# Performance work log

Hardware: AMD Instinct MI355X
Metric: run time of the kernel (lower is better)

The kernel has to match this reference:

```python
import jax, jax.numpy as jnp
import numpy as np

N_STEPS = 4  # fixed-step dopri5 substeps over [t0, t1]
T0, T1 = 0.0, 1.0
EPS = 1e-5

# Dormand-Prince 5(4) Butcher tableau (5th-order solution weights)
_DP_A = [
    [],
    [1/5],
    [3/40, 9/40],
    [44/45, -56/15, 32/9],
    [19372/6561, -25360/2187, 64448/6561, -212/729],
    [9017/3168, -355/33, 46732/5247, 49/176, -5103/18656],
    [35/384, 0.0, 500/1113, 125/192, -2187/6784, 11/84],
]
_DP_B = [35/384, 0.0, 500/1113, 125/192, -2187/6784, 11/84, 0.0]


def _layernorm(x, g, b):
    mu = jnp.mean(x, axis=-1, keepdims=True)
    var = jnp.var(x, axis=-1, keepdims=True)
    return (x - mu) * jax.lax.rsqrt(var + EPS) * g + b


def build_laplacian(edge_index, edge_attr, num_nodes, ew_w1, ew_b1, ew_w2, ew_b2):
    # learnable edge weights: Linear(1,32) -> ReLU -> Linear(32,1) -> Sigmoid
    h = jax.nn.relu(edge_attr @ ew_w1 + ew_b1)            # [E,32]
    ew = jax.nn.sigmoid(h @ ew_w2 + ew_b2)[:, 0]           # [E]
    row, col = edge_index[0], edge_index[1]
    # add self loops with weight 1
    loop = jnp.arange(num_nodes, dtype=edge_index.dtype)
    row = jnp.concatenate([row, loop])
    col = jnp.concatenate([col, loop])
    ew = jnp.concatenate([ew, jnp.ones((num_nodes,), dtype=ew.dtype)])
    # degree counts edges incident on col (unweighted, as torch_geometric.degree)
    deg = jnp.zeros((num_nodes,), dtype=ew.dtype).at[col].add(1.0)
    dis = jnp.where(deg > 0, deg ** -0.5, 0.0)
    w = dis[row] * ew * dis[col]
    adj = jnp.zeros((num_nodes, num_nodes), dtype=ew.dtype).at[row, col].add(w)
    return jnp.eye(num_nodes, dtype=ew.dtype) - adj


def ode_func(state, L, context, p):
    # state: [B,N,F], L: [N,N], context: [B,F]
    B, N, F = state.shape
    ctx = jnp.broadcast_to(context[:, None, :], (B, N, F))
    x = jnp.concatenate([state, ctx], axis=-1)             # [B,N,2F]
    h = jax.nn.relu(_layernorm(x @ p['td_w1'] + p['td_b1'], p['ln1_g'], p['ln1_b']))
    h = jax.nn.relu(_layernorm(h @ p['td_w2'] + p['td_b2'], p['ln2_g'], p['ln2_b']))
    dhdt_temporal = h @ p['td_w3'] + p['td_b3']            # [B,N,F]
    dcoef = jax.nn.sigmoid(jax.nn.relu(state @ p['df_w1'] + p['df_b1']) @ p['df_w2'] + p['df_b2'])  # [B,N,1]
    Lh = jnp.einsum('ij,bjf->bif', L, state)               # batched diffusion
    return dhdt_temporal - dcoef * Lh


def dopri5_fixed(f, y0, t0, t1, n_steps):
    dt = (t1 - t0) / n_steps

    def step(y, _):
        ks = []
        for i in range(7):
            yi = y
            for j, aij in enumerate(_DP_A[i]):
                if aij != 0.0:
                    yi = yi + dt * aij * ks[j]
            ks.append(f(yi))
        ynew = y
        for bi, ki in zip(_DP_B, ks):
            if bi != 0.0:
                ynew = ynew + dt * bi * ki
        return ynew, None

    y, _ = jax.lax.scan(step, y0, None, length=n_steps)
    return y


def setup_inputs() -> dict:
    key = jax.random.key(0)
    ks = jax.random.split(key, 24)
    B, N, F, H, E = 4, 2048, 256, 512, 65536
    s = lambda k, *shape: jax.random.normal(k, shape, dtype=jnp.float32) * 0.05
    return {
        'state': jax.random.normal(ks[0], (B, N, F), dtype=jnp.float32),
        'context': jax.random.normal(ks[1], (B, F), dtype=jnp.float32),
        'edge_attr': jax.random.uniform(ks[2], (E, 1), dtype=jnp.float32),
        'edge_index': jax.random.randint(ks[3], (2, E), 0, N, dtype=jnp.int32),
        'ew_w1': s(ks[4], 1, 32), 'ew_b1': jnp.zeros((32,), jnp.float32),
        'ew_w2': s(ks[5], 32, 1), 'ew_b2': jnp.zeros((1,), jnp.float32),
        'td_w1': s(ks[6], 2 * F, H), 'td_b1': jnp.zeros((H,), jnp.float32),
        'ln1_g': jnp.ones((H,), jnp.float32), 'ln1_b': jnp.zeros((H,), jnp.float32),
        'td_w2': s(ks[7], H, H), 'td_b2': jnp.zeros((H,), jnp.float32),
        'ln2_g': jnp.ones((H,), jnp.float32), 'ln2_b': jnp.zeros((H,), jnp.float32),
        'td_w3': s(ks[8], H, F), 'td_b3': jnp.zeros((F,), jnp.float32),
        'df_w1': s(ks[9], F, H // 2), 'df_b1': jnp.zeros((H // 2,), jnp.float32),
        'df_w2': s(ks[10], H // 2, 1), 'df_b2': jnp.zeros((1,), jnp.float32),
    }


def reference(state, context, edge_attr, edge_index,
              ew_w1, ew_b1, ew_w2, ew_b2,
              td_w1, td_b1, ln1_g, ln1_b, td_w2, td_b2, ln2_g, ln2_b, td_w3, td_b3,
              df_w1, df_b1, df_w2, df_b2):
    N = state.shape[1]
    L = build_laplacian(edge_index, edge_attr, N, ew_w1, ew_b1, ew_w2, ew_b2)
    p = dict(td_w1=td_w1, td_b1=td_b1, ln1_g=ln1_g, ln1_b=ln1_b,
             td_w2=td_w2, td_b2=td_b2, ln2_g=ln2_g, ln2_b=ln2_b,
             td_w3=td_w3, td_b3=td_b3, df_w1=df_w1, df_b1=df_b1,
             df_w2=df_w2, df_b2=df_b2)
    f = lambda y: ode_func(y, L, context, p)
    return dopri5_fixed(f, state, T0, T1, N_STEPS)
```

## Files before the change

### kernel.cpp

```cpp
#include <hip/hip_runtime.h>
#include <cstddef>
#include <cstdint>

#define N_NODES 2048
#define BATCH   4
#define FDIM    256
#define HDIM    512
#define NEDGE   65536
#define BN_     8192
#define DT      0.25f

typedef __attribute__((ext_vector_type(8))) __bf16 bf16x8;
typedef __attribute__((ext_vector_type(4))) float f32x4;

__device__ __forceinline__ ushort f2bf(float f) {
    union { float f; unsigned u; } v; v.f = f;
    return (ushort)((v.u + 0x7FFF + ((v.u >> 16) & 1)) >> 16);
}
__device__ __forceinline__ float bf2f(ushort u) {
    union { float f; unsigned u; } v; v.u = ((unsigned)u) << 16; return v.f;
}
__device__ __forceinline__ void gload16(const void* g, void* l) {
    __builtin_amdgcn_global_load_lds((const __attribute__((address_space(1))) void*)g,
                                     (__attribute__((address_space(3))) void*)l, 16, 0, 0);
}

__global__ void edge_ew_deg(const float* __restrict__ attr, const int* __restrict__ eidx,
                            const float* __restrict__ w1, const float* __restrict__ b1,
                            const float* __restrict__ w2, const float* __restrict__ b2,
                            float* __restrict__ ew, float* __restrict__ deg) {
    int e = blockIdx.x * blockDim.x + threadIdx.x;
    if (e >= NEDGE) return;
    float a = attr[e];
    float s = b2[0];
#pragma unroll
    for (int k = 0; k < 32; ++k)
        s += fmaxf(fmaf(a, w1[k], b1[k]), 0.f) * w2[k];
    ew[e] = 1.f / (1.f + expf(-s));
    atomicAdd(&deg[eidx[NEDGE + e]], 1.f);
}

__global__ void dis_diag(const float* __restrict__ deg, float* __restrict__ dis,
                         float* __restrict__ L) {
    int n = blockIdx.x * blockDim.x + threadIdx.x;
    if (n >= N_NODES) return;
    float d = deg[n] + 1.f;
    dis[n] = rsqrtf(d);
    L[(size_t)n * N_NODES + n] = 1.f - 1.f / d;
}

__global__ void scatter_L(const int* __restrict__ eidx, const float* __restrict__ ew,
                          const float* __restrict__ dis, float* __restrict__ L) {
    int e = blockIdx.x * blockDim.x + threadIdx.x;
    if (e >= NEDGE) return;
    int r = eidx[e], c = eidx[NEDGE + e];
    atomicAdd(&L[(size_t)r * N_NODES + c], -dis[r] * ew[e] * dis[c]);
}

__global__ void ctxproj_kernel(const float* __restrict__ ctx, const float* __restrict__ w1,
                               const float* __restrict__ b1, float* __restrict__ out) {
    int b = blockIdx.x, h = threadIdx.x;
    const float* W = w1 + (size_t)FDIM * HDIM + h;
    const float* c = ctx + b * FDIM;
    float s = b1[h];
#pragma unroll 4
    for (int k = 0; k < FDIM; ++k)
        s = fmaf(c[k], W[(size_t)k * HDIM], s);
    out[b * HDIM + h] = s;
}

__global__ __launch_bounds__(256)
void transpose_cvt(const float* __restrict__ in, int inStride, ushort* __restrict__ out,
                   int R, int C) {
    __shared__ float tile[64][65];
    int r0 = blockIdx.x * 64, c0 = blockIdx.y * 64;
    int t = threadIdx.x, tr = t >> 4, tc = t & 15;
#pragma unroll
    for (int i = 0; i < 4; ++i) {
        float4 v = *(const float4*)&in[(size_t)(r0 + tr + i * 16) * inStride + c0 + tc * 4];
        tile[tr + i * 16][tc * 4 + 0] = v.x; tile[tr + i * 16][tc * 4 + 1] = v.y;
        tile[tr + i * 16][tc * 4 + 2] = v.z; tile[tr + i * 16][tc * 4 + 3] = v.w;
    }
    __syncthreads();
#pragma unroll
    for (int i = 0; i < 4; ++i) {
        int c = tr + i * 16;
        ushort4 o = make_ushort4(f2bf(tile[tc * 4 + 0][c]), f2bf(tile[tc * 4 + 1][c]),
                                 f2bf(tile[tc * 4 + 2][c]), f2bf(tile[tc * 4 + 3][c]));
        *(ushort4*)&out[(size_t)(c0 + c) * R + r0 + tc * 4] = o;
    }
}

__global__ void cvt_bf16(const float* __restrict__ in, ushort* __restrict__ out) {
    int i = blockIdx.x * blockDim.x + threadIdx.x;
    float4 v = ((const float4*)in)[i];
    ((ushort4*)out)[i] = make_ushort4(f2bf(v.x), f2bf(v.y), f2bf(v.z), f2bf(v.w));
}

__global__ __launch_bounds__(256)
void combine_all(const float* __restrict__ base,
                 const ushort* p0, const ushort* p1, const ushort* p2,
                 const ushort* p3, const ushort* p4,
                 float c0, float c1, float c2, float c3, float c4,
                 float* __restrict__ dstf, ushort* __restrict__ yi,
                 ushort* __restrict__ yiT) {
    __shared__ ushort tile[64][68];
    int nb = blockIdx.x * 64, fb = blockIdx.y * 64, b = blockIdx.z;
    int t = threadIdx.x, tr = t >> 4, tc = t & 15;
#pragma unroll
    for (int i = 0; i < 4; ++i) {
        int nl = tr + i * 16;
        size_t fi = (((size_t)(b * N_NODES + nb + nl) * FDIM) + fb + tc * 4) >> 2;
        float4 v = ((const float4*)base)[fi];
        if (p0) { ushort4 q = ((const ushort4*)p0)[fi]; v.x = fmaf(c0,bf2f(q.x),v.x); v.y = fmaf(c0,bf2f(q.y),v.y); v.z = fmaf(c0,bf2f(q.z),v.z); v.w = fmaf(c0,bf2f(q.w),v.w); }
        if (p1) { ushort4 q = ((const ushort4*)p1)[fi]; v.x = fmaf(c1,bf2f(q.x),v.x); v.y = fmaf(c1,bf2f(q.y),v.y); v.z = fmaf(c1,bf2f(q.z),v.z); v.w = fmaf(c1,bf2f(q.w),v.w); }
        if (p2) { ushort4 q = ((const ushort4*)p2)[fi]; v.x = fmaf(c2,bf2f(q.x),v.x); v.y = fmaf(c2,bf2f(q.y),v.y); v.z = fmaf(c2,bf2f(q.z),v.z); v.w = fmaf(c2,bf2f(q.w),v.w); }
        if (p3) { ushort4 q = ((const ushort4*)p3)[fi]; v.x = fmaf(c3,bf2f(q.x),v.x); v.y = fmaf(c3,bf2f(q.y),v.y); v.z = fmaf(c3,bf2f(q.z),v.z); v.w = fmaf(c3,bf2f(q.w),v.w); }
        if (p4) { ushort4 q = ((const ushort4*)p4)[fi]; v.x = fmaf(c4,bf2f(q.x),v.x); v.y = fmaf(c4,bf2f(q.y),v.y); v.z = fmaf(c4,bf2f(q.z),v.z); v.w = fmaf(c4,bf2f(q.w),v.w); }
        if (dstf) ((float4*)dstf)[fi] = v;
        ushort4 o = make_ushort4(f2bf(v.x), f2bf(v.y), f2bf(v.z), f2bf(v.w));
        if (yi) ((ushort4*)yi)[fi] = o;
        tile[nl][tc * 4 + 0] = o.x; tile[nl][tc * 4 + 1] = o.y;
        tile[nl][tc * 4 + 2] = o.z; tile[nl][tc * 4 + 3] = o.w;
    }
    __syncthreads();
    if (!yiT) return;
#pragma unroll
    for (int i = 0; i < 4; ++i) {
        int fl = tr + i * 16;
        ushort4 o = make_ushort4(tile[tc * 4 + 0][fl], tile[tc * 4 + 1][fl],
                                 tile[tc * 4 + 2][fl], tile[tc * 4 + 3][fl]);
        *(ushort4*)&yiT[((size_t)(b * FDIM + fb + fl) * N_NODES) + nb + tc * 4] = o;
    }
}

template<int BM, int BN, int BK, int WM, int WN, int BIAS, int EPI>
__global__ __launch_bounds__(256)
void gemm(const ushort* __restrict__ A, const ushort* __restrict__ BT,
          const float* __restrict__ bias, const float* __restrict__ bias2,
          void* __restrict__ C, int N, int K, long sA, long sB, long sC) {
    constexpr int MR  = BM / WM / 16;
    constexpr int NR  = BN / WN / 16;
    constexpr int CPR = BK / 8;
    constexpr int ALD = BM * CPR / 256;
    constexpr int BLD = BN * CPR / 256;
    constexpr int KK  = BK / 32;
    __shared__ ushort As[BM * BK];
    __shared__ ushort Bs[BN * BK];
    const ushort* Ag = A + (size_t)blockIdx.z * sA;
    const ushort* Bg = BT + (size_t)blockIdx.z * sB;
    const int tid = threadIdx.x;
    const int lane = tid & 63, wid = tid >> 6;
    const int wn = wid % WN, wm = wid / WN;
    const int r15 = lane & 15, g = lane >> 4;
    const int rowBase = blockIdx.y * BM, colBase = blockIdx.x * BN;

    f32x4 acc[MR][NR];
#pragma unroll
    for (int m = 0; m < MR; ++m)
#pragma unroll
        for (int n = 0; n < NR; ++n) acc[m][n] = (f32x4){0.f, 0.f, 0.f, 0.f};

    for (int k0 = 0; k0 < K; k0 += BK) {
#pragma unroll
        for (int c = 0; c < ALD; ++c) {
            int ci = (wid * ALD + c) * 64 + lane;
            int row = ci / CPR, ch = ci % CPR;
            gload16(Ag + (size_t)(rowBase + row) * K + k0 + ((ch ^ (row & 7)) << 3),
                    &As[((wid * ALD + c) * 64) * 8]);
        }
#pragma unroll
        for (int c = 0; c < BLD; ++c) {
            int ci = (wid * BLD + c) * 64 + lane;
            int row = ci / CPR, ch = ci % CPR;
            gload16(Bg + (size_t)(colBase + row) * K + k0 + ((ch ^ (row & 7)) << 3),
                    &Bs[((wid * BLD + c) * 64) * 8]);
        }
        __syncthreads();
#pragma unroll
        for (int kk = 0; kk < KK; ++kk) {
            bf16x8 af[MR], bfr[NR];
#pragma unroll
            for (int m = 0; m < MR; ++m) {
                int lr = wm * (BM / WM) + m * 16 + r15;
                int off = lr * (BK * 2) + ((kk * 64 + g * 16) ^ ((lr & 7) << 4));
                af[m] = *(const bf16x8*)((const char*)As + off);
            }
#pragma unroll
            for (int n = 0; n < NR; ++n) {
                int br = wn * (BN / WN) + n * 16 + r15;
                int off = br * (BK * 2) + ((kk * 64 + g * 16) ^ ((br & 7) << 4));
                bfr[n] = *(const bf16x8*)((const char*)Bs + off);
            }
#pragma unroll
            for (int m = 0; m < MR; ++m)
#pragma unroll
                for (int n = 0; n < NR; ++n)
                    acc[m][n] = __builtin_amdgcn_mfma_f32_16x16x32_bf16(
                        af[m], bfr[n], acc[m][n], 0, 0, 0);
        }
        __syncthreads();
    }
    if (EPI == 2) {
        int b = colBase >> 8;
        ushort* ks = (ushort*)C;
#pragma unroll
        for (int m = 0; m < MR; ++m) {
            int row = rowBase + wm * (BM / WM) + m * 16 + g * 4;
            float4 dcv = *(const float4*)&bias2[b * N_NODES + row];
            float dca[4] = {dcv.x, dcv.y, dcv.z, dcv.w};
#pragma unroll
            for (int n = 0; n < NR; ++n) {
                int col = colBase + wn * (BN / WN) + n * 16 + r15;
                int f = col & 255;
#pragma unroll
                for (int r = 0; r < 4; ++r) {
                    size_t idx = ((size_t)(b * N_NODES + row + r)) * 256 + f;
                    ks[idx] = f2bf(bf2f(ks[idx]) - dca[r] * acc[m][n][r]);
                }
            }
        }
        return;
    }
#pragma unroll
    for (int m = 0; m < MR; ++m) {
        int row = rowBase + wm * (BM / WM) + m * 16 + g * 4;
#pragma unroll
        for (int n = 0; n < NR; ++n) {
            int col = colBase + wn * (BN / WN) + n * 16 + r15;
            float bv = 0.f;
            if (BIAS == 1) bv = bias[col];
            if (BIAS == 3) bv = (col < HDIM) ? bias[(row >> 11) * HDIM + col]
                                             : bias2[col - HDIM];
#pragma unroll
            for (int r = 0; r < 4; ++r) {
                float v = acc[m][n][r] + bv;
                if (EPI == 1) ((ushort*)C)[(size_t)blockIdx.z * sC + (size_t)(row + r) * N + col] = f2bf(v);
                else          ((float*)C)[(size_t)blockIdx.z * sC + (size_t)(row + r) * N + col] = v;
            }
        }
    }
}

__global__ __launch_bounds__(256)
void ln_dc_768(const ushort* __restrict__ hcat, ushort* __restrict__ out,
               const float* __restrict__ g, const float* __restrict__ b,
               const float* __restrict__ w2, const float* __restrict__ b2,
               float* __restrict__ dc) {
    int row = blockIdx.x, t = threadIdx.x;
    const ushort* hrow = hcat + (size_t)row * 768;
    unsigned u = *(const unsigned*)&hrow[2 * t];
    float v0 = bf2f((ushort)(u & 0xffff)), v1 = bf2f((ushort)(u >> 16));
    float d = fmaxf(bf2f(hrow[512 + t]), 0.f) * w2[t];
    float s = v0 + v1, s2 = v0 * v0 + v1 * v1;
#pragma unroll
    for (int o = 32; o > 0; o >>= 1) {
        s += __shfl_down(s, o); s2 += __shfl_down(s2, o); d += __shfl_down(d, o);
    }
    __shared__ float red[12];
    int w = t >> 6;
    if ((t & 63) == 0) { red[w] = s; red[4 + w] = s2; red[8 + w] = d; }
    __syncthreads();
    s  = red[0] + red[1] + red[2] + red[3];
    s2 = red[4] + red[5] + red[6] + red[7];
    if (t == 0) {
        float dd = red[8] + red[9] + red[10] + red[11];
        dc[row] = 1.f / (1.f + expf(-(dd + b2[0])));
    }
    float mu  = s * (1.f / HDIM);
    float var = fmaf(-mu, mu, s2 * (1.f / HDIM));
    float inv = rsqrtf(var + 1e-5f);
    float n0 = fmaxf(fmaf((v0 - mu) * inv, g[2 * t],     b[2 * t]),     0.f);
    float n1 = fmaxf(fmaf((v1 - mu) * inv, g[2 * t + 1], b[2 * t + 1]), 0.f);
    *(unsigned*)&out[(size_t)row * HDIM + 2 * t] =
        (unsigned)f2bf(n0) | ((unsigned)f2bf(n1) << 16);
}

template<int IS>
__global__ __launch_bounds__(256)
void ln_bf(const ushort* __restrict__ in, ushort* __restrict__ out,
           const float* __restrict__ g, const float* __restrict__ b) {
    int row = blockIdx.x, t = threadIdx.x;
    unsigned u = *(const unsigned*)&in[(size_t)row * IS + 2 * t];
    float v0 = bf2f((ushort)(u & 0xffff)), v1 = bf2f((ushort)(u >> 16));
    float s = v0 + v1, s2 = v0 * v0 + v1 * v1;
#pragma unroll
    for (int o = 32; o > 0; o >>= 1) { s += __shfl_down(s, o); s2 += __shfl_down(s2, o); }
    __shared__ float red[8];
    int w = t >> 6;
    if ((t & 63) == 0) { red[w] = s; red[4 + w] = s2; }
    __syncthreads();
    s  = red[0] + red[1] + red[2] + red[3];
    s2 = red[4] + red[5] + red[6] + red[7];
    float mu  = s * (1.f / HDIM);
    float var = fmaf(-mu, mu, s2 * (1.f / HDIM));
    float inv = rsqrtf(var + 1e-5f);
    float n0 = fmaxf(fmaf((v0 - mu) * inv, g[2 * t],     b[2 * t]),     0.f);
    float n1 = fmaxf(fmaf((v1 - mu) * inv, g[2 * t + 1], b[2 * t + 1]), 0.f);
    *(unsigned*)&out[(size_t)row * HDIM + 2 * t] =
        (unsigned)f2bf(n0) | ((unsigned)f2bf(n1) << 16);
}

extern "C" void kernel_launch(void* const* d_in, const int* in_sizes, int n_in,
                              void* d_out, int out_size, void* d_ws, size_t ws_size,
                              hipStream_t stream) {
    const float* state      = (const float*)d_in[0];
    const float* context    = (const float*)d_in[1];
    const float* edge_attr  = (const float*)d_in[2];
    const int*   edge_index = (const int*)d_in[3];
    const float* ew_w1 = (const float*)d_in[4];
    const float* ew_b1 = (const float*)d_in[5];
    const float* ew_w2 = (const float*)d_in[6];
    const float* ew_b2 = (const float*)d_in[7];
    const float* td_w1 = (const float*)d_in[8];
    const float* td_b1 = (const float*)d_in[9];
    const float* ln1_g = (const float*)d_in[10];
    const float* ln1_b = (const float*)d_in[11];
    const float* td_w2 = (const float*)d_in[12];
    const float* td_b2 = (const float*)d_in[13];
    const float* ln2_g = (const float*)d_in[14];
    const float* ln2_b = (const float*)d_in[15];
    const float* td_w3 = (const float*)d_in[16];
    const float* td_b3 = (const float*)d_in[17];
    const float* df_w1 = (const float*)d_in[18];
    const float* df_b1 = (const float*)d_in[19];
    const float* df_w2 = (const float*)d_in[20];
    const float* df_b2 = (const float*)d_in[21];
    float* out = (float*)d_out;

    float* ws = (float*)d_ws;
    size_t off = 0;
    auto alloc = [&](size_t nfloats) { float* p = ws + off; off += nfloats; return p; };
    float*  ew    = alloc(NEDGE);
    float*  deg   = alloc(N_NODES);
    float*  dis   = alloc(N_NODES);
    float*  ctxp  = alloc((size_t)BATCH * HDIM);
    float*  dc    = alloc(BN_);
    float*  L     = alloc((size_t)N_NODES * N_NODES);
    ushort* Lbf   = (ushort*)alloc((size_t)N_NODES * N_NODES / 2);
    float*  y     = alloc((size_t)BN_ * FDIM);
    ushort* yi    = (ushort*)alloc((size_t)BN_ * FDIM / 2);
    ushort* yiT   = (ushort*)alloc((size_t)BN_ * FDIM / 2);
    ushort* hcat  = (ushort*)alloc((size_t)BN_ * 768 / 2);
    ushort* hb1   = (ushort*)alloc((size_t)BN_ * HDIM / 2);
    ushort* h2b   = (ushort*)alloc((size_t)BN_ * HDIM / 2);
    ushort* wcat  = (ushort*)alloc((size_t)768 * FDIM / 2);
    ushort* w2T   = (ushort*)alloc((size_t)HDIM * HDIM / 2);
    ushort* w3T   = (ushort*)alloc((size_t)FDIM * HDIM / 2);
    ushort* kb[6];
    for (int s = 0; s < 6; ++s) kb[s] = (ushort*)alloc((size_t)BN_ * FDIM / 2);

    hipMemsetAsync(deg, 0, N_NODES * sizeof(float), stream);
    hipMemsetAsync(L, 0, (size_t)N_NODES * N_NODES * sizeof(float), stream);
    edge_ew_deg<<<NEDGE / 256, 256, 0, stream>>>(edge_attr, edge_index, ew_w1, ew_b1, ew_w2, ew_b2, ew, deg);
    dis_diag<<<N_NODES / 256, 256, 0, stream>>>(deg, dis, L);
    scatter_L<<<NEDGE / 256, 256, 0, stream>>>(edge_index, ew, dis, L);
    cvt_bf16<<<(N_NODES * N_NODES / 4) / 256, 256, 0, stream>>>(L, Lbf);
    ctxproj_kernel<<<BATCH, HDIM, 0, stream>>>(context, td_w1, td_b1, ctxp);
    transpose_cvt<<<dim3(FDIM / 64, HDIM / 64), 256, 0, stream>>>(td_w1, HDIM, wcat, FDIM, HDIM);
    transpose_cvt<<<dim3(FDIM / 64, FDIM / 64), 256, 0, stream>>>(df_w1, FDIM, wcat + (size_t)HDIM * FDIM, FDIM, FDIM);
    transpose_cvt<<<dim3(HDIM / 64, HDIM / 64), 256, 0, stream>>>(td_w2, HDIM, w2T, HDIM, HDIM);
    transpose_cvt<<<dim3(HDIM / 64, FDIM / 64), 256, 0, stream>>>(td_w3, FDIM, w3T, HDIM, FDIM);

    static const double DPA[6][5] = {
        {0, 0, 0, 0, 0},
        {1.0/5, 0, 0, 0, 0},
        {3.0/40, 9.0/40, 0, 0, 0},
        {44.0/45, -56.0/15, 32.0/9, 0, 0},
        {19372.0/6561, -25360.0/2187, 64448.0/6561, -212.0/729, 0},
        {9017.0/3168, -355.0/33, 46732.0/5247, 49.0/176, -5103.0/18656},
    };

    const dim3 cgrid(N_NODES / 64, FDIM / 64, BATCH);
    const float* ycur = state;
    for (int step = 0; step < 4; ++step) {
        for (int s = 0; s < 6; ++s) {
            if (s == 0) {
                if (step == 0)
                    combine_all<<<cgrid, 256, 0, stream>>>(ycur, nullptr, nullptr, nullptr,
                        nullptr, nullptr, 0, 0, 0, 0, 0, nullptr, yi, yiT);
            } else {
                const ushort* p[5] = {nullptr, nullptr, nullptr, nullptr, nullptr};
                float c[5] = {0, 0, 0, 0, 0};
                for (int j = 0; j < s; ++j) { p[j] = kb[j]; c[j] = (float)(DT * DPA[s][j]); }
                combine_all<<<cgrid, 256, 0, stream>>>(ycur, p[0], p[1], p[2], p[3], p[4],
                    c[0], c[1], c[2], c[3], c[4], nullptr, yi, yiT);
            }
            ushort* ks = kb[s];
            gemm<128, 128, 64, 2, 2, 3, 1><<<dim3(768 / 128, BN_ / 128, 1), 256, 0, stream>>>(
                yi, wcat, ctxp, df_b1, hcat, 768, FDIM, 0, 0, 0);
            ln_dc_768<<<BN_, 256, 0, stream>>>(hcat, hb1, ln1_g, ln1_b, df_w2, df_b2, dc);
            gemm<64, 128, 128, 1, 4, 1, 1><<<dim3(HDIM / 128, BN_ / 64, 1), 256, 0, stream>>>(
                hb1, w2T, td_b2, nullptr, h2b, HDIM, HDIM, 0, 0, 0);
            ln_bf<512><<<BN_, 256, 0, stream>>>(h2b, h2b, ln2_g, ln2_b);
            gemm<64, 64, 128, 2, 2, 1, 1><<<dim3(FDIM / 64, BN_ / 64, 1), 256, 0, stream>>>(
                h2b, w3T, td_b3, nullptr, ks, FDIM, HDIM, 0, 0, 0);
            gemm<64, 64, 128, 2, 2, 0, 2><<<dim3(1024 / 64, N_NODES / 64, 1), 256, 0, stream>>>(
                Lbf, yiT, nullptr, dc, ks, 1024, N_NODES, 0, 0, 0);
        }
        float* dstf = (step == 3) ? out : y;
        combine_all<<<cgrid, 256, 0, stream>>>(ycur,
            kb[0], kb[2], kb[3], kb[4], kb[5],
            (float)(DT * 35.0 / 384), (float)(DT * 500.0 / 1113), (float)(DT * 125.0 / 192),
            (float)(DT * -2187.0 / 6784), (float)(DT * 11.0 / 84),
            dstf, (step == 3) ? nullptr : yi, (step == 3) ? nullptr : yiT);
        ycur = y;
    }
    (void)in_sizes; (void)n_in; (void)out_size; (void)ws_size;
}
```

Measured before the change: 1.973 ms.

## Fuse LayerNorm+ReLU prologue into the following GEMMs via LDS-resident A rows

Replaces the standalone LayerNorm kernels (ln_dc_768, ln_bf) and the two GEMMs that consumed their output with a gemm_ln kernel. It loads a full 64-row A tile (all K) into LDS, computes row mean/variance, normalizes with ReLU in place, and also computes the diffusion coefficient, then runs the MFMA GEMM. This removes two kernel launches per stage and the write/read round trip of the normalized intermediate. In exchange, each column block recomputes the LayerNorm for its rows, the kernel uses a large LDS footprint that may reduce occupancy, and the B loads are not double-buffered.

```diff
diff --git a/kernel.cpp b/kernel.cpp
--- a/kernel.cpp
+++ b/kernel.cpp
@@ -242,63 +242,151 @@
     }
 }
 
+template<int KF, int ASTR, int BN, int BK, int DCF>
 __global__ __launch_bounds__(256)
-void ln_dc_768(const ushort* __restrict__ hcat, ushort* __restrict__ out,
-               const float* __restrict__ g, const float* __restrict__ b,
-               const float* __restrict__ w2, const float* __restrict__ b2,
-               float* __restrict__ dc) {
-    int row = blockIdx.x, t = threadIdx.x;
-    const ushort* hrow = hcat + (size_t)row * 768;
-    unsigned u = *(const unsigned*)&hrow[2 * t];
-    float v0 = bf2f((ushort)(u & 0xffff)), v1 = bf2f((ushort)(u >> 16));
-    float d = fmaxf(bf2f(hrow[512 + t]), 0.f) * w2[t];
-    float s = v0 + v1, s2 = v0 * v0 + v1 * v1;
-#pragma unroll
-    for (int o = 32; o > 0; o >>= 1) {
-        s += __shfl_down(s, o); s2 += __shfl_down(s2, o); d += __shfl_down(d, o);
-    }
-    __shared__ float red[12];
-    int w = t >> 6;
-    if ((t & 63) == 0) { red[w] = s; red[4 + w] = s2; red[8 + w] = d; }
+void gemm_ln(const ushort* __restrict__ A, const ushort* __restrict__ BT,
+             const float* __restrict__ lng, const float* __restrict__ lnb,
+             const float* __restrict__ bias,
+             const float* __restrict__ w2, const float* __restrict__ b2,
+             float* __restrict__ dcout, ushort* __restrict__ C, int N) {
+    constexpr int CPR  = KF / 8;
+    constexpr int AIT  = 64 * CPR / 256;
+    constexpr int BCPR = BK / 8;
+    constexpr int BIT  = BN * BCPR / 256;
+    constexpr int KK   = BK / 32;
+    constexpr int MR = 2, NR = BN / 2 / 16;
+    __shared__ ushort As[64 * KF];
+    __shared__ ushort Bs[BN * BK];
+    const int tid = threadIdx.x;
+    const int lane = tid & 63, wid = tid >> 6;
+    const int wn = wid & 1, wm = wid >> 1;
+    const int r15 = lane & 15, g = lane >> 4;
+    const int rowBase = blockIdx.y * 64, colBase = blockIdx.x * BN;
+
+#pragma unroll
+    for (int c = 0; c < AIT; ++c) {
+        int base = c * 256 + wid * 64;
+        int ci = base + lane;
+        int row = ci / CPR, ch = ci % CPR;
+        gload16(A + (size_t)(rowBase + row) * ASTR + ((ch ^ (row & 7)) << 3),
+                &As[base * 8]);
+    }
     __syncthreads();
-    s  = red[0] + red[1] + red[2] + red[3];
-    s2 = red[4] + red[5] + red[6] + red[7];
-    if (t == 0) {
-        float dd = red[8] + red[9] + red[10] + red[11];
-        dc[row] = 1.f / (1.f + expf(-(dd + b2[0])));
-    }
-    float mu  = s * (1.f / HDIM);
-    float var = fmaf(-mu, mu, s2 * (1.f / HDIM));
-    float inv = rsqrtf(var + 1e-5f);
-    float n0 = fmaxf(fmaf((v0 - mu) * inv, g[2 * t],     b[2 * t]),     0.f);
-    float n1 = fmaxf(fmaf((v1 - mu) * inv, g[2 * t + 1], b[2 * t + 1]), 0.f);
-    *(unsigned*)&out[(size_t)row * HDIM + 2 * t] =
-        (unsigned)f2bf(n0) | ((unsigned)f2bf(n1) << 16);
-}
-
-template<int IS>
-__global__ __launch_bounds__(256)
-void ln_bf(const ushort* __restrict__ in, ushort* __restrict__ out,
-           const float* __restrict__ g, const float* __restrict__ b) {
-    int row = blockIdx.x, t = threadIdx.x;
-    unsigned u = *(const unsigned*)&in[(size_t)row * IS + 2 * t];
-    float v0 = bf2f((ushort)(u & 0xffff)), v1 = bf2f((ushort)(u >> 16));
-    float s = v0 + v1, s2 = v0 * v0 + v1 * v1;
-#pragma unroll
-    for (int o = 32; o > 0; o >>= 1) { s += __shfl_down(s, o); s2 += __shfl_down(s2, o); }
-    __shared__ float red[8];
-    int w = t >> 6;
-    if ((t & 63) == 0) { red[w] = s; red[4 + w] = s2; }
+
+    {
+        const int row = tid >> 2, q = tid & 3;
+        const int c0 = q * (CPR / 4), c1 = c0 + CPR / 4;
+        float s = 0.f, s2 = 0.f;
+        for (int ch = c0; ch < c1; ++ch) {
+            uint4 pk = *(const uint4*)&As[row * KF + ch * 8];
+            float x0 = bf2f((ushort)(pk.x & 0xffff)), x1 = bf2f((ushort)(pk.x >> 16));
+            float x2 = bf2f((ushort)(pk.y & 0xffff)), x3 = bf2f((ushort)(pk.y >> 16));
+            float x4 = bf2f((ushort)(pk.z & 0xffff)), x5 = bf2f((ushort)(pk.z >> 16));
+            float x6 = bf2f((ushort)(pk.w & 0xffff)), x7 = bf2f((ushort)(pk.w >> 16));
+            s  += (x0 + x1) + (x2 + x3) + (x4 + x5) + (x6 + x7);
+            s2 += (x0*x0 + x1*x1) + (x2*x2 + x3*x3) + (x4*x4 + x5*x5) + (x6*x6 + x7*x7);
+        }
+        float d = 0.f;
+        if (DCF) {
+            const ushort* hr = A + (size_t)(rowBase + row) * ASTR + 512 + q * 64;
+#pragma unroll
+            for (int j = 0; j < 8; ++j) {
+                uint4 pk = *(const uint4*)&hr[j * 8];
+                const float* wv = w2 + q * 64 + j * 8;
+                d += fmaxf(bf2f((ushort)(pk.x & 0xffff)), 0.f) * wv[0]
+                   + fmaxf(bf2f((ushort)(pk.x >> 16)),    0.f) * wv[1]
+                   + fmaxf(bf2f((ushort)(pk.y & 0xffff)), 0.f) * wv[2]
+                   + fmaxf(bf2f((ushort)(pk.y >> 16)),    0.f) * wv[3]
+                   + fmaxf(bf2f((ushort)(pk.z & 0xffff)), 0.f) * wv[4]
+                   + fmaxf(bf2f((ushort)(pk.z >> 16)),    0.f) * wv[5]
+                   + fmaxf(bf2f((ushort)(pk.w & 0xffff)), 0.f) * wv[6]
+                   + fmaxf(bf2f((ushort)(pk.w >> 16)),    0.f) * wv[7];
+            }
+        }
+        s  += __shfl_xor(s, 1);  s  += __shfl_xor(s, 2);
+        s2 += __shfl_xor(s2, 1); s2 += __shfl_xor(s2, 2);
+        if (DCF) {
+            d += __shfl_xor(d, 1); d += __shfl_xor(d, 2);
+            if (q == 0 && blockIdx.x == 0)
+                dcout[rowBase + row] = 1.f / (1.f + expf(-(d + b2[0])));
+        }
+        float mu  = s * (1.f / KF);
+        float inv = rsqrtf(fmaf(-mu, mu, s2 * (1.f / KF)) + 1e-5f);
+        for (int ch = c0; ch < c1; ++ch) {
+            int gk = (ch ^ (row & 7)) * 8;
+            uint4 pk = *(const uint4*)&As[row * KF + ch * 8];
+            float4 ga = *(const float4*)&lng[gk], gb = *(const float4*)&lng[gk + 4];
+            float4 ba = *(const float4*)&lnb[gk], bb = *(const float4*)&lnb[gk + 4];
+            float v0 = fmaxf(fmaf((bf2f((ushort)(pk.x & 0xffff)) - mu) * inv, ga.x, ba.x), 0.f);
+            float v1 = fmaxf(fmaf((bf2f((ushort)(pk.x >> 16))    - mu) * inv, ga.y, ba.y), 0.f);
+            float v2 = fmaxf(fmaf((bf2f((ushort)(pk.y & 0xffff)) - mu) * inv, ga.z, ba.z), 0.f);
+            float v3 = fmaxf(fmaf((bf2f((ushort)(pk.y >> 16))    - mu) * inv, ga.w, ba.w), 0.f);
+            float v4 = fmaxf(fmaf((bf2f((ushort)(pk.z & 0xffff)) - mu) * inv, gb.x, bb.x), 0.f);
+            float v5 = fmaxf(fmaf((bf2f((ushort)(pk.z >> 16))    - mu) * inv, gb.y, bb.y), 0.f);
+            float v6 = fmaxf(fmaf((bf2f((ushort)(pk.w & 0xffff)) - mu) * inv, gb.z, bb.z), 0.f);
+            float v7 = fmaxf(fmaf((bf2f((ushort)(pk.w >> 16))    - mu) * inv, gb.w, bb.w), 0.f);
+            uint4 o;
+            o.x = (unsigned)f2bf(v0) | ((unsigned)f2bf(v1) << 16);
+            o.y = (unsigned)f2bf(v2) | ((unsigned)f2bf(v3) << 16);
+            o.z = (unsigned)f2bf(v4) | ((unsigned)f2bf(v5) << 16);
+            o.w = (unsigned)f2bf(v6) | ((unsigned)f2bf(v7) << 16);
+            *(uint4*)&As[row * KF + ch * 8] = o;
+        }
+    }
     __syncthreads();
-    s  = red[0] + red[1] + red[2] + red[3];
-    s2 = red[4] + red[5] + red[6] + red[7];
-    float mu  = s * (1.f / HDIM);
-    float var = fmaf(-mu, mu, s2 * (1.f / HDIM));
-    float inv = rsqrtf(var + 1e-5f);
-    float n0 = fmaxf(fmaf((v0 - mu) * inv, g[2 * t],     b[2 * t]),     0.f);
-    float n1 = fmaxf(fmaf((v1 - mu) * inv, g[2 * t + 1], b[2 * t + 1]), 0.f);
-    *(unsigned*)&out[(size_t)row * HDIM + 2 * t] =
-        (unsigned)f2bf(n0) | ((unsigned)f2bf(n1) << 16);
+
+    f32x4 acc[MR][NR];
+#pragma unroll
+    for (int m = 0; m < MR; ++m)
+#pragma unroll
+        for (int n = 0; n < NR; ++n) acc[m][n] = (f32x4){0.f, 0.f, 0.f, 0.f};
+
+    for (int k0 = 0; k0 < KF; k0 += BK) {
+#pragma unroll
+        for (int c = 0; c < BIT; ++c) {
+            int base = c * 256 + wid * 64;
+            int ci = base + lane;
+            int row = ci / BCPR, ch = ci % BCPR;
+            gload16(BT + (size_t)(colBase + row) * KF + k0 + ((ch ^ (row & 7)) << 3),
+                    &Bs[base * 8]);
+        }
+        __syncthreads();
+#pragma unroll
+        for (int kk = 0; kk < KK; ++kk) {
+            bf16x8 af[MR], bfr[NR];
+#pragma unroll
+            for (int m = 0; m < MR; ++m) {
+                int lr = wm * 32 + m * 16 + r15;
+                int off = lr * (KF * 2) + ((k0 * 2 + kk * 64 + g * 16) ^ ((lr & 7) << 4));
+                af[m] = *(const bf16x8*)((const char*)As + off);
+            }
+#pragma unroll
+            for (int n = 0; n < NR; ++n) {
+                int br = wn * (BN / 2) + n * 16 + r15;
+                int off = br * (BK * 2) + ((kk * 64 + g * 16) ^ ((br & 7) << 4));
+                bfr[n] = *(const bf16x8*)((const char*)Bs + off);
+            }
+#pragma unroll
+            for (int m = 0; m < MR; ++m)
+#pragma unroll
+                for (int n = 0; n < NR; ++n)
+                    acc[m][n] = __builtin_amdgcn_mfma_f32_16x16x32_bf16(
+                        af[m], bfr[n], acc[m][n], 0, 0, 0);
+        }
+        __syncthreads();
+    }
+#pragma unroll
+    for (int m = 0; m < MR; ++m) {
+        int row = rowBase + wm * 32 + m * 16 + g * 4;
+#pragma unroll
+        for (int n = 0; n < NR; ++n) {
+            int col = colBase + wn * (BN / 2) + n * 16 + r15;
+            float bv = bias[col];
+#pragma unroll
+            for (int r = 0; r < 4; ++r)
+                C[(size_t)(row + r) * N + col] = f2bf(acc[m][n][r] + bv);
+        }
+    }
 }
 
 extern "C" void kernel_launch(void* const* d_in, const int* in_sizes, int n_in,
@@ -342,7 +430,6 @@
     ushort* yi    = (ushort*)alloc((size_t)BN_ * FDIM / 2);
     ushort* yiT   = (ushort*)alloc((size_t)BN_ * FDIM / 2);
     ushort* hcat  = (ushort*)alloc((size_t)BN_ * 768 / 2);
-    ushort* hb1   = (ushort*)alloc((size_t)BN_ * HDIM / 2);
     ushort* h2b   = (ushort*)alloc((size_t)BN_ * HDIM / 2);
     ushort* wcat  = (ushort*)alloc((size_t)768 * FDIM / 2);
     ushort* w2T   = (ushort*)alloc((size_t)HDIM * HDIM / 2);
@@ -389,12 +476,10 @@
             ushort* ks = kb[s];
             gemm<128, 128, 64, 2, 2, 3, 1><<<dim3(768 / 128, BN_ / 128, 1), 256, 0, stream>>>(
                 yi, wcat, ctxp, df_b1, hcat, 768, FDIM, 0, 0, 0);
-            ln_dc_768<<<BN_, 256, 0, stream>>>(hcat, hb1, ln1_g, ln1_b, df_w2, df_b2, dc);
-            gemm<64, 128, 128, 1, 4, 1, 1><<<dim3(HDIM / 128, BN_ / 64, 1), 256, 0, stream>>>(
-                hb1, w2T, td_b2, nullptr, h2b, HDIM, HDIM, 0, 0, 0);
-            ln_bf<512><<<BN_, 256, 0, stream>>>(h2b, h2b, ln2_g, ln2_b);
-            gemm<64, 64, 128, 2, 2, 1, 1><<<dim3(FDIM / 64, BN_ / 64, 1), 256, 0, stream>>>(
-                h2b, w3T, td_b3, nullptr, ks, FDIM, HDIM, 0, 0, 0);
+            gemm_ln<512, 768, 64, 128, 1><<<dim3(HDIM / 64, BN_ / 64), 256, 0, stream>>>(
+                hcat, w2T, ln1_g, ln1_b, td_b2, df_w2, df_b2, dc, h2b, HDIM);
+            gemm_ln<512, 512, 64, 128, 0><<<dim3(FDIM / 64, BN_ / 64), 256, 0, stream>>>(
+                h2b, w3T, ln2_g, ln2_b, td_b3, nullptr, nullptr, nullptr, ks, FDIM);
             gemm<64, 64, 128, 2, 2, 0, 2><<<dim3(1024 / 64, N_NODES / 64, 1), 256, 0, stream>>>(
                 Lbf, yiT, nullptr, dc, ks, 1024, N_NODES, 0, 0, 0);
         }
```

Result: slower. 3.348 ms (+69.7%).
